# Kernel tuning notes

Hardware: AMD Instinct MI355X
Metric: run time of the kernel (lower is better)

Reference implementation:

```python
import jax, jax.numpy as jnp
import numpy as np

L = 65536   # sequence length (keys/values)
D = 512     # embed dim (hardcoded in source)
H = 4       # heads
HD = 128    # head dim

def _ln(x, g, b):
    m = jnp.mean(x, -1, keepdims=True)
    v = jnp.var(x, -1, keepdims=True)
    return (x - m) * jax.lax.rsqrt(v + 1e-5) * g + b

def setup_inputs() -> dict:
    key = jax.random.key(0)
    ks = jax.random.split(key, 6)
    s = 0.02
    return {
        "x": jax.random.normal(ks[0], (L, D), jnp.float32),
        "w_in": jax.random.normal(ks[1], (3 * D, D), jnp.float32) * s,
        "b_in": jnp.zeros((3 * D,), jnp.float32),
        "w_out": jax.random.normal(ks[2], (D, D), jnp.float32) * s,
        "b_out": jnp.zeros((D,), jnp.float32),
        "w1": jax.random.normal(ks[3], (D, D), jnp.float32) * s,
        "b1": jnp.zeros((D,), jnp.float32),
        "w2": jax.random.normal(ks[4], (D, D), jnp.float32) * s,
        "b2": jnp.zeros((D,), jnp.float32),
        "g1": jnp.ones((D,), jnp.float32),
        "be1": jnp.zeros((D,), jnp.float32),
        "g2": jnp.ones((D,), jnp.float32),
        "be2": jnp.zeros((D,), jnp.float32),
    }

def reference(x, w_in, b_in, w_out, b_out, w1, b1, w2, b2, g1, be1, g2, be2):
    xn = _ln(x, g1, be1)                               # [L, D]
    q = xn[:1] @ w_in[:D].T + b_in[:D]                 # [1, D] single-row query
    k = xn @ w_in[D:2 * D].T + b_in[D:2 * D]           # [L, D]
    v = xn @ w_in[2 * D:].T + b_in[2 * D:]             # [L, D]
    qh = q.reshape(H, HD)                              # [H, HD]
    kh = k.reshape(L, H, HD)
    vh = v.reshape(L, H, HD)
    scores = jnp.einsum('hd,lhd->hl', qh, kh) * (1.0 / np.sqrt(HD))  # [H, L]
    attn = jax.nn.softmax(scores, axis=-1)
    o = jnp.einsum('hl,lhd->hd', attn, vh).reshape(1, D)             # [1, D]
    o = o @ w_out.T + b_out
    y = x[:1] + o                                      # residual keeps only row 0
    yn = _ln(y, g2, be2)
    h = jax.nn.relu(yn @ w1.T + b1)
    return y + h @ w2.T + b2                           # [1, D]
```

## Files before the change

### kernel.cpp

```cpp
#include <hip/hip_runtime.h>
#include <math.h>

#define LL 65536
#define DD 512
#define NH 4
#define HDIM 128


__device__ __forceinline__ float dot4(float4 a, float4 b) {
    return a.x * b.x + a.y * b.y + a.z * b.z + a.w * b.w;
}
__device__ __forceinline__ float wred(float v) {
#pragma unroll
    for (int m = 32; m; m >>= 1) v += __shfl_xor(v, m, 64);
    return v;
}
__device__ __forceinline__ float4 f4fma(float4 acc, float s, float4 v) {
    acc.x += s * v.x; acc.y += s * v.y; acc.z += s * v.z; acc.w += s * v.w;
    return acc;
}
__device__ __forceinline__ float4 f4add(float4 a, float4 b) {
    a.x += b.x; a.y += b.y; a.z += b.z; a.w += b.w; return a;
}
__device__ __forceinline__ float4 f4muls(float4 a, float4 g, float s) {
    a.x *= g.x * s; a.y *= g.y * s; a.z *= g.z * s; a.w *= g.w * s; return a;
}
__device__ __forceinline__ float hsum4(float4 a) { return a.x + a.y + a.z + a.w; }
__device__ __forceinline__ float4 lnrm4(float4 v, float m, float r, float4 g, float4 b) {
    float4 o;
    o.x = (v.x - m) * r * g.x + b.x; o.y = (v.y - m) * r * g.y + b.y;
    o.z = (v.z - m) * r * g.z + b.z; o.w = (v.w - m) * r * g.w + b.w;
    return o;
}
__device__ __forceinline__ float4 caff4(float4 c, float inv, float w2t, float4 g, float4 b) {
    float4 o;
    o.x = g.x * (c.x * inv - w2t) + b.x; o.y = g.y * (c.y * inv - w2t) + b.y;
    o.z = g.z * (c.z * inv - w2t) + b.z; o.w = g.w * (c.w * inv - w2t) + b.w;
    return o;
}

__global__ __launch_bounds__(256) void kA1(const float* __restrict__ x,
                                           const float* __restrict__ w_in,
                                           const float* __restrict__ b_in,
                                           const float* __restrict__ g1,
                                           const float* __restrict__ be1,
                                           float* __restrict__ ws) {
    int lane = threadIdx.x & 63;
    int j = blockIdx.x * 4 + (threadIdx.x >> 6);
    const float4* x4 = (const float4*)x;
    float4 a = x4[lane], b = x4[64 + lane];
    float ps = hsum4(a) + hsum4(b);
    float pss = dot4(a, a) + dot4(b, b);
    ps = wred(ps); pss = wred(pss);
    float m = ps * (1.f / 512.f);
    float r = rsqrtf(pss * (1.f / 512.f) - m * m + 1e-5f);
    const float4* g4 = (const float4*)g1;
    const float4* bb4 = (const float4*)be1;
    float4 xna = lnrm4(a, m, r, g4[lane], bb4[lane]);
    float4 xnb = lnrm4(b, m, r, g4[64 + lane], bb4[64 + lane]);
    const float4* wr = (const float4*)(w_in + (size_t)j * DD);
    float acc = dot4(wr[lane], xna) + dot4(wr[64 + lane], xnb);
    acc = wred(acc);
    if (lane == 0) ws[j] = acc + b_in[j];
}

__global__ __launch_bounds__(512) void kA2(const float* __restrict__ w_in,
                                           float* __restrict__ ws) {
    __shared__ float qh[32];
    int bi = blockIdx.x, tid = threadIdx.x;
    int h = bi >> 2, c = bi & 3;
    if (tid < 32) qh[tid] = ws[h * HDIM + c * 32 + tid];
    if (tid < 128) ws[9216 + bi * 128 + tid] = 0.f;
    __syncthreads();
    const float* wk = w_in + (size_t)(DD + h * HDIM + c * 32) * DD + tid;
    float acc = 0.f;
#pragma unroll
    for (int d = 0; d < 32; ++d) acc += qh[d] * wk[(size_t)d * DD];
    ws[1024 + c * 2048 + h * 512 + tid] = acc;
}

__global__ __launch_bounds__(512) void kB(const float* __restrict__ x,
                                          const float* __restrict__ g1,
                                          float* __restrict__ ws) {
    __shared__ float lds[16384];
    int tid = threadIdx.x, lane = tid & 63, w = tid >> 6;
    const float4* p4 = (const float4*)(ws + 1024);
    const float4* g4 = (const float4*)g1;
    const float scale = 0.088388347648318447f;
    float4 ga = g4[lane], gb = g4[64 + lane];
    float4 qa[4], qb[4];
    float qs[4];
#pragma unroll
    for (int h = 0; h < 4; ++h) {
        float4 sa = f4add(f4add(p4[h * 128 + lane], p4[512 + h * 128 + lane]),
                          f4add(p4[1024 + h * 128 + lane], p4[1536 + h * 128 + lane]));
        float4 sb = f4add(f4add(p4[h * 128 + 64 + lane], p4[512 + h * 128 + 64 + lane]),
                          f4add(p4[1024 + h * 128 + 64 + lane], p4[1536 + h * 128 + 64 + lane]));
        qa[h] = f4muls(sa, ga, scale);
        qb[h] = f4muls(sb, gb, scale);
        qs[h] = wred(hsum4(qa[h]) + hsum4(qb[h]));
    }
    float sm[4], w2a[4];
    float4 Wa[4], Wb[4];
#pragma unroll
    for (int h = 0; h < 4; ++h) {
        sm[h] = 0.f; w2a[h] = 0.f;
        Wa[h] = make_float4(0.f, 0.f, 0.f, 0.f);
        Wb[h] = make_float4(0.f, 0.f, 0.f, 0.f);
    }
    size_t row0 = ((size_t)blockIdx.x * 8 + w) * 16;
    const float4* xb = (const float4*)x + row0 * 128;
    float4 nxa = xb[lane], nxc = xb[64 + lane];
    for (int r = 0; r < 16; ++r) {
        float4 xa = nxa, xc = nxc;
        if (r < 15) { nxa = xb[(r + 1) * 128 + lane]; nxc = xb[(r + 1) * 128 + 64 + lane]; }
        float ps = hsum4(xa) + hsum4(xc);
        float pss = dot4(xa, xa) + dot4(xc, xc);
        float p0 = dot4(xa, qa[0]) + dot4(xc, qb[0]);
        float p1 = dot4(xa, qa[1]) + dot4(xc, qb[1]);
        float p2 = dot4(xa, qa[2]) + dot4(xc, qb[2]);
        float p3 = dot4(xa, qa[3]) + dot4(xc, qb[3]);
        ps = wred(ps); pss = wred(pss);
        p0 = wred(p0); p1 = wred(p1); p2 = wred(p2); p3 = wred(p3);
        float m = ps * (1.f / 512.f);
        float rr = rsqrtf(pss * (1.f / 512.f) - m * m + 1e-5f);
        float rm = rr * m;
        float pd[4] = {p0, p1, p2, p3};
#pragma unroll
        for (int h = 0; h < 4; ++h) {
            float s = rr * pd[h] - rm * qs[h];
            float p = __expf(s);
            sm[h] += p;
            w2a[h] += p * rm;
            float pr = p * rr;
            Wa[h] = f4fma(Wa[h], pr, xa);
            Wb[h] = f4fma(Wb[h], pr, xc);
        }
    }
    if (lane == 0) {
#pragma unroll
        for (int h = 0; h < 4; ++h) {
            lds[w * 4 + h] = sm[h];
            lds[32 + w * 4 + h] = w2a[h];
        }
    }
    __syncthreads();
    if (tid < 8) {
        int h = tid & 3;
        float a = 0.f;
        if (tid < 4) {
            for (int ww = 0; ww < 8; ++ww) a += lds[ww * 4 + h];
            ws[16384 + blockIdx.x * 4 + h] = a;
        } else {
            for (int ww = 0; ww < 8; ++ww) a += lds[32 + ww * 4 + h];
            ws[18432 + blockIdx.x * 4 + h] = a;
        }
    }
    __syncthreads();
    float4* lw4 = (float4*)(lds + w * 2048);
#pragma unroll
    for (int h = 0; h < 4; ++h) {
        lw4[h * 128 + lane] = Wa[h];
        lw4[h * 128 + 64 + lane] = Wb[h];
    }
    __syncthreads();
    float* Wout = ws + 20480 + (size_t)blockIdx.x * 2048;
    for (int i = tid; i < 2048; i += 512) {
        float a = lds[i] + lds[2048 + i] + lds[4096 + i] + lds[6144 + i] +
                  lds[8192 + i] + lds[10240 + i] + lds[12288 + i] + lds[14336 + i];
        Wout[i] = a;
    }
}

__global__ __launch_bounds__(256) void kC1(float* __restrict__ ws) {
    int g = blockIdx.x * 256 + threadIdx.x;
    int col = g & 2047, chunk = g >> 11;
    const float* Wb = ws + 20480 + (size_t)chunk * 32 * 2048 + col;
    float acc = 0.f;
#pragma unroll 8
    for (int b = 0; b < 32; ++b) acc += Wb[(size_t)b * 2048];
    atomicAdd(&ws[9216 + col], acc);
}

__global__ __launch_bounds__(256) void kD1(const float* __restrict__ w_in,
                                           const float* __restrict__ b_in,
                                           const float* __restrict__ g1,
                                           const float* __restrict__ be1,
                                           float* __restrict__ ws) {
    __shared__ float sred[16];
    int tid = threadIdx.x, lane = tid & 63, w = tid >> 6;
    int j = blockIdx.x * 4 + w;
    int h = j >> 7;
    float s1 = ws[16384 + tid * 4 + h] + ws[16384 + (tid + 256) * 4 + h];
    float s2 = ws[18432 + tid * 4 + h] + ws[18432 + (tid + 256) * 4 + h];
    s1 = wred(s1); s2 = wred(s2);
    if (lane == 0) { sred[w * 2] = s1; sred[w * 2 + 1] = s2; }
    __syncthreads();
    float smg = sred[0] + sred[2] + sred[4] + sred[6];
    float w2g = sred[1] + sred[3] + sred[5] + sred[7];
    float inv = 1.f / smg;
    float w2t = w2g * inv;
    const float4* cr = (const float4*)(ws + 9216 + h * 512);
    const float4* g14 = (const float4*)g1;
    const float4* be14 = (const float4*)be1;
    float4 ca = caff4(cr[lane], inv, w2t, g14[lane], be14[lane]);
    float4 cb = caff4(cr[64 + lane], inv, w2t, g14[64 + lane], be14[64 + lane]);
    const float4* wr = (const float4*)(w_in + (size_t)(2 * DD + j) * DD);
    float acc = dot4(wr[lane], ca) + dot4(wr[64 + lane], cb);
    acc = wred(acc);
    if (lane == 0) ws[11264 + j] = acc + b_in[2 * DD + j];
}

__global__ __launch_bounds__(256) void kD2(const float* __restrict__ x,
                                           const float* __restrict__ w_out,
                                           const float* __restrict__ b_out,
                                           float* __restrict__ ws) {
    int lane = threadIdx.x & 63;
    int j = blockIdx.x * 4 + (threadIdx.x >> 6);
    const float4* wr = (const float4*)(w_out + (size_t)j * DD);
    const float4* o4 = (const float4*)(ws + 11264);
    float acc = dot4(wr[lane], o4[lane]) + dot4(wr[64 + lane], o4[64 + lane]);
    acc = wred(acc);
    if (lane == 0) ws[11776 + j] = x[j] + acc + b_out[j];
}

__global__ __launch_bounds__(256) void kD3(const float* __restrict__ w1,
                                           const float* __restrict__ b1,
                                           const float* __restrict__ g2,
                                           const float* __restrict__ be2,
                                           float* __restrict__ ws) {
    int lane = threadIdx.x & 63;
    int j = blockIdx.x * 4 + (threadIdx.x >> 6);
    const float4* y4 = (const float4*)(ws + 11776);
    float4 ya = y4[lane], yb = y4[64 + lane];
    float ps = hsum4(ya) + hsum4(yb);
    float pss = dot4(ya, ya) + dot4(yb, yb);
    ps = wred(ps); pss = wred(pss);
    float m2 = ps * (1.f / 512.f);
    float r2 = rsqrtf(pss * (1.f / 512.f) - m2 * m2 + 1e-5f);
    const float4* g4 = (const float4*)g2;
    const float4* b4 = (const float4*)be2;
    float4 yna = lnrm4(ya, m2, r2, g4[lane], b4[lane]);
    float4 ynb = lnrm4(yb, m2, r2, g4[64 + lane], b4[64 + lane]);
    const float4* wr = (const float4*)(w1 + (size_t)j * DD);
    float acc = dot4(wr[lane], yna) + dot4(wr[64 + lane], ynb);
    acc = wred(acc);
    if (lane == 0) ws[12288 + j] = fmaxf(acc + b1[j], 0.f);
}

__global__ __launch_bounds__(256) void kD4(const float* __restrict__ w2,
                                           const float* __restrict__ b2,
                                           const float* __restrict__ ws,
                                           float* __restrict__ out) {
    int lane = threadIdx.x & 63;
    int j = blockIdx.x * 4 + (threadIdx.x >> 6);
    const float4* h4 = (const float4*)(ws + 12288);
    const float4* wr = (const float4*)(w2 + (size_t)j * DD);
    float acc = dot4(wr[lane], h4[lane]) + dot4(wr[64 + lane], h4[64 + lane]);
    acc = wred(acc);
    if (lane == 0) out[j] = ws[11776 + j] + acc + b2[j];
}

extern "C" void kernel_launch(void* const* d_in, const int* in_sizes, int n_in,
                              void* d_out, int out_size, void* d_ws, size_t ws_size,
                              hipStream_t stream) {
    (void)in_sizes; (void)n_in; (void)out_size; (void)ws_size;
    const float* x = (const float*)d_in[0];
    const float* w_in = (const float*)d_in[1];
    const float* b_in = (const float*)d_in[2];
    const float* w_out = (const float*)d_in[3];
    const float* b_out = (const float*)d_in[4];
    const float* w1 = (const float*)d_in[5];
    const float* b1 = (const float*)d_in[6];
    const float* w2 = (const float*)d_in[7];
    const float* b2 = (const float*)d_in[8];
    const float* g1 = (const float*)d_in[9];
    const float* be1 = (const float*)d_in[10];
    const float* g2 = (const float*)d_in[11];
    const float* be2 = (const float*)d_in[12];
    float* ws = (float*)d_ws;
    float* out = (float*)d_out;

    hipLaunchKernelGGL(kA1, dim3(128), dim3(256), 0, stream, x, w_in, b_in, g1, be1, ws);
    hipLaunchKernelGGL(kA2, dim3(16), dim3(512), 0, stream, w_in, ws);
    hipLaunchKernelGGL(kB, dim3(512), dim3(512), 0, stream, x, g1, ws);
    hipLaunchKernelGGL(kC1, dim3(128), dim3(256), 0, stream, ws);
    hipLaunchKernelGGL(kD1, dim3(128), dim3(256), 0, stream, w_in, b_in, g1, be1, ws);
    hipLaunchKernelGGL(kD2, dim3(128), dim3(256), 0, stream, x, w_out, b_out, ws);
    hipLaunchKernelGGL(kD3, dim3(128), dim3(256), 0, stream, w1, b1, g2, be2, ws);
    hipLaunchKernelGGL(kD4, dim3(128), dim3(256), 0, stream, w2, b2, ws, out);
}
```

Measured before the change: 239.1 us.

## Fuse all stages into one cooperative kernel with grid-wide syncs

Replaces the eight separate kernel launches with one cooperative kernel of 256 blocks that uses grid.sync between phases. The first phase now computes q and the q·Wk product in just 4 blocks. The main streaming pass does 32 rows per warp with a two-deep prefetch. Partial sums are reduced through LDS and atomics into 8 slot buffers, which removes the separate cross-block reduction kernel. This cuts launch and inter-kernel gaps, at the cost of grid barriers, heavier serial work in a few blocks for the first phase, and atomic contention.

Measured after the change: 417.5 us. 74.6% more time.

```diff
diff --git a/kernel.cpp b/kernel.cpp
--- a/kernel.cpp
+++ b/kernel.cpp
@@ -1,10 +1,10 @@
 #include <hip/hip_runtime.h>
+#include <hip/hip_cooperative_groups.h>
 #include <math.h>
 
-#define LL 65536
+namespace cg = cooperative_groups;
+
 #define DD 512
-#define NH 4
-#define HDIM 128
 
 
 __device__ __forceinline__ float dot4(float4 a, float4 b) {
@@ -21,9 +21,6 @@
 }
 __device__ __forceinline__ float4 f4add(float4 a, float4 b) {
     a.x += b.x; a.y += b.y; a.z += b.z; a.w += b.w; return a;
-}
-__device__ __forceinline__ float4 f4muls(float4 a, float4 g, float s) {
-    a.x *= g.x * s; a.y *= g.y * s; a.z *= g.z * s; a.w *= g.w * s; return a;
 }
 __device__ __forceinline__ float hsum4(float4 a) { return a.x + a.y + a.z + a.w; }
 __device__ __forceinline__ float4 lnrm4(float4 v, float m, float r, float4 g, float4 b) {
@@ -39,226 +36,222 @@
     return o;
 }
 
-__global__ __launch_bounds__(256) void kA1(const float* __restrict__ x,
-                                           const float* __restrict__ w_in,
-                                           const float* __restrict__ b_in,
-                                           const float* __restrict__ g1,
-                                           const float* __restrict__ be1,
-                                           float* __restrict__ ws) {
-    int lane = threadIdx.x & 63;
-    int j = blockIdx.x * 4 + (threadIdx.x >> 6);
-    const float4* x4 = (const float4*)x;
-    float4 a = x4[lane], b = x4[64 + lane];
-    float ps = hsum4(a) + hsum4(b);
-    float pss = dot4(a, a) + dot4(b, b);
-    ps = wred(ps); pss = wred(pss);
-    float m = ps * (1.f / 512.f);
-    float r = rsqrtf(pss * (1.f / 512.f) - m * m + 1e-5f);
-    const float4* g4 = (const float4*)g1;
-    const float4* bb4 = (const float4*)be1;
-    float4 xna = lnrm4(a, m, r, g4[lane], bb4[lane]);
-    float4 xnb = lnrm4(b, m, r, g4[64 + lane], bb4[64 + lane]);
-    const float4* wr = (const float4*)(w_in + (size_t)j * DD);
-    float acc = dot4(wr[lane], xna) + dot4(wr[64 + lane], xnb);
-    acc = wred(acc);
-    if (lane == 0) ws[j] = acc + b_in[j];
-}
-
-__global__ __launch_bounds__(512) void kA2(const float* __restrict__ w_in,
-                                           float* __restrict__ ws) {
-    __shared__ float qh[32];
-    int bi = blockIdx.x, tid = threadIdx.x;
-    int h = bi >> 2, c = bi & 3;
-    if (tid < 32) qh[tid] = ws[h * HDIM + c * 32 + tid];
-    if (tid < 128) ws[9216 + bi * 128 + tid] = 0.f;
-    __syncthreads();
-    const float* wk = w_in + (size_t)(DD + h * HDIM + c * 32) * DD + tid;
-    float acc = 0.f;
-#pragma unroll
-    for (int d = 0; d < 32; ++d) acc += qh[d] * wk[(size_t)d * DD];
-    ws[1024 + c * 2048 + h * 512 + tid] = acc;
-}
-
-__global__ __launch_bounds__(512) void kB(const float* __restrict__ x,
-                                          const float* __restrict__ g1,
-                                          float* __restrict__ ws) {
-    __shared__ float lds[16384];
+__global__ __launch_bounds__(512, 2) void kMega(
+    const float* __restrict__ x,
+    const float* __restrict__ w_in, const float* __restrict__ b_in,
+    const float* __restrict__ w_out, const float* __restrict__ b_out,
+    const float* __restrict__ w1, const float* __restrict__ b1,
+    const float* __restrict__ w2, const float* __restrict__ b2,
+    const float* __restrict__ g1, const float* __restrict__ be1,
+    const float* __restrict__ g2, const float* __restrict__ be2,
+    float* __restrict__ ws, float* __restrict__ out)
+{
+    __shared__ float lds[8192];
+    __shared__ float lstats[64];
+    cg::grid_group grid = cg::this_grid();
     int tid = threadIdx.x, lane = tid & 63, w = tid >> 6;
-    const float4* p4 = (const float4*)(ws + 1024);
-    const float4* g4 = (const float4*)g1;
+    int bid = blockIdx.x;
     const float scale = 0.088388347648318447f;
-    float4 ga = g4[lane], gb = g4[64 + lane];
-    float4 qa[4], qb[4];
-    float qs[4];
-#pragma unroll
-    for (int h = 0; h < 4; ++h) {
-        float4 sa = f4add(f4add(p4[h * 128 + lane], p4[512 + h * 128 + lane]),
-                          f4add(p4[1024 + h * 128 + lane], p4[1536 + h * 128 + lane]));
-        float4 sb = f4add(f4add(p4[h * 128 + 64 + lane], p4[512 + h * 128 + 64 + lane]),
-                          f4add(p4[1024 + h * 128 + 64 + lane], p4[1536 + h * 128 + 64 + lane]));
-        qa[h] = f4muls(sa, ga, scale);
-        qb[h] = f4muls(sb, gb, scale);
-        qs[h] = wred(hsum4(qa[h]) + hsum4(qb[h]));
-    }
-    float sm[4], w2a[4];
-    float4 Wa[4], Wb[4];
-#pragma unroll
-    for (int h = 0; h < 4; ++h) {
-        sm[h] = 0.f; w2a[h] = 0.f;
-        Wa[h] = make_float4(0.f, 0.f, 0.f, 0.f);
-        Wb[h] = make_float4(0.f, 0.f, 0.f, 0.f);
-    }
-    size_t row0 = ((size_t)blockIdx.x * 8 + w) * 16;
-    const float4* xb = (const float4*)x + row0 * 128;
-    float4 nxa = xb[lane], nxc = xb[64 + lane];
-    for (int r = 0; r < 16; ++r) {
-        float4 xa = nxa, xc = nxc;
-        if (r < 15) { nxa = xb[(r + 1) * 128 + lane]; nxc = xb[(r + 1) * 128 + 64 + lane]; }
-        float ps = hsum4(xa) + hsum4(xc);
-        float pss = dot4(xa, xa) + dot4(xc, xc);
-        float p0 = dot4(xa, qa[0]) + dot4(xc, qb[0]);
-        float p1 = dot4(xa, qa[1]) + dot4(xc, qb[1]);
-        float p2 = dot4(xa, qa[2]) + dot4(xc, qb[2]);
-        float p3 = dot4(xa, qa[3]) + dot4(xc, qb[3]);
-        ps = wred(ps); pss = wred(pss);
-        p0 = wred(p0); p1 = wred(p1); p2 = wred(p2); p3 = wred(p3);
+
+    if (bid < 4) {
+        int h = bid;
+        const float4* x4 = (const float4*)x;
+        float4 a = x4[lane], b = x4[64 + lane];
+        float ps = wred(hsum4(a) + hsum4(b));
+        float pss = wred(dot4(a, a) + dot4(b, b));
         float m = ps * (1.f / 512.f);
-        float rr = rsqrtf(pss * (1.f / 512.f) - m * m + 1e-5f);
-        float rm = rr * m;
-        float pd[4] = {p0, p1, p2, p3};
+        float r = rsqrtf(pss * (1.f / 512.f) - m * m + 1e-5f);
+        const float4* g4 = (const float4*)g1;
+        const float4* bb4 = (const float4*)be1;
+        float4 xna = lnrm4(a, m, r, g4[lane], bb4[lane]);
+        float4 xnb = lnrm4(b, m, r, g4[64 + lane], bb4[64 + lane]);
+        const float4* wr = (const float4*)(w_in + (size_t)(h * 128 + w * 16) * DD);
+        float4 wa = wr[lane], wb = wr[64 + lane];
+        for (int i = 0; i < 16; ++i) {
+            float4 ca = wa, cb = wb;
+            if (i < 15) { wa = wr[(i + 1) * 128 + lane]; wb = wr[(i + 1) * 128 + 64 + lane]; }
+            float acc = wred(dot4(ca, xna) + dot4(cb, xnb));
+            if (lane == 0) lds[w * 16 + i] = acc + b_in[h * 128 + w * 16 + i];
+        }
+        __syncthreads();
+        const float* wk = w_in + (size_t)(DD + h * 128) * DD + tid;
+        float acc = 0.f;
+#pragma unroll 16
+        for (int d = 0; d < 128; ++d) acc += lds[d] * wk[(size_t)d * DD];
+        float qg = acc * scale * g1[tid];
+        ws[h * 512 + tid] = qg;
+        float s = wred(qg);
+        if (lane == 0) lds[4096 + w] = s;
+        __syncthreads();
+        if (tid == 0) {
+            float t = 0.f;
+            for (int ww = 0; ww < 8; ++ww) t += lds[4096 + ww];
+            ws[2048 + h] = t;
+        }
+    } else if (bid < 36) {
+        ws[4096 + (bid - 4) * 512 + tid] = 0.f;
+        if (bid == 35 && tid < 192) ws[2176 + tid] = 0.f;
+    }
+    grid.sync();
+
+    {
+        const float4* qkg4 = (const float4*)ws;
+        float4 qa[4], qb[4];
+        float qs[4];
 #pragma unroll
         for (int h = 0; h < 4; ++h) {
-            float s = rr * pd[h] - rm * qs[h];
-            float p = __expf(s);
-            sm[h] += p;
-            w2a[h] += p * rm;
-            float pr = p * rr;
-            Wa[h] = f4fma(Wa[h], pr, xa);
-            Wb[h] = f4fma(Wb[h], pr, xc);
-        }
-    }
-    if (lane == 0) {
+            qa[h] = qkg4[h * 128 + lane];
+            qb[h] = qkg4[h * 128 + 64 + lane];
+            qs[h] = ws[2048 + h];
+        }
+        float sm[4], w2a[4];
+        float4 Wa[4], Wb[4];
 #pragma unroll
         for (int h = 0; h < 4; ++h) {
-            lds[w * 4 + h] = sm[h];
-            lds[32 + w * 4 + h] = w2a[h];
-        }
-    }
-    __syncthreads();
-    if (tid < 8) {
-        int h = tid & 3;
-        float a = 0.f;
-        if (tid < 4) {
-            for (int ww = 0; ww < 8; ++ww) a += lds[ww * 4 + h];
-            ws[16384 + blockIdx.x * 4 + h] = a;
-        } else {
-            for (int ww = 0; ww < 8; ++ww) a += lds[32 + ww * 4 + h];
-            ws[18432 + blockIdx.x * 4 + h] = a;
-        }
-    }
-    __syncthreads();
-    float4* lw4 = (float4*)(lds + w * 2048);
-#pragma unroll
-    for (int h = 0; h < 4; ++h) {
-        lw4[h * 128 + lane] = Wa[h];
-        lw4[h * 128 + 64 + lane] = Wb[h];
-    }
-    __syncthreads();
-    float* Wout = ws + 20480 + (size_t)blockIdx.x * 2048;
-    for (int i = tid; i < 2048; i += 512) {
-        float a = lds[i] + lds[2048 + i] + lds[4096 + i] + lds[6144 + i] +
-                  lds[8192 + i] + lds[10240 + i] + lds[12288 + i] + lds[14336 + i];
-        Wout[i] = a;
-    }
-}
-
-__global__ __launch_bounds__(256) void kC1(float* __restrict__ ws) {
-    int g = blockIdx.x * 256 + threadIdx.x;
-    int col = g & 2047, chunk = g >> 11;
-    const float* Wb = ws + 20480 + (size_t)chunk * 32 * 2048 + col;
-    float acc = 0.f;
-#pragma unroll 8
-    for (int b = 0; b < 32; ++b) acc += Wb[(size_t)b * 2048];
-    atomicAdd(&ws[9216 + col], acc);
-}
-
-__global__ __launch_bounds__(256) void kD1(const float* __restrict__ w_in,
-                                           const float* __restrict__ b_in,
-                                           const float* __restrict__ g1,
-                                           const float* __restrict__ be1,
-                                           float* __restrict__ ws) {
-    __shared__ float sred[16];
-    int tid = threadIdx.x, lane = tid & 63, w = tid >> 6;
-    int j = blockIdx.x * 4 + w;
-    int h = j >> 7;
-    float s1 = ws[16384 + tid * 4 + h] + ws[16384 + (tid + 256) * 4 + h];
-    float s2 = ws[18432 + tid * 4 + h] + ws[18432 + (tid + 256) * 4 + h];
-    s1 = wred(s1); s2 = wred(s2);
-    if (lane == 0) { sred[w * 2] = s1; sred[w * 2 + 1] = s2; }
-    __syncthreads();
-    float smg = sred[0] + sred[2] + sred[4] + sred[6];
-    float w2g = sred[1] + sred[3] + sred[5] + sred[7];
-    float inv = 1.f / smg;
-    float w2t = w2g * inv;
-    const float4* cr = (const float4*)(ws + 9216 + h * 512);
-    const float4* g14 = (const float4*)g1;
-    const float4* be14 = (const float4*)be1;
-    float4 ca = caff4(cr[lane], inv, w2t, g14[lane], be14[lane]);
-    float4 cb = caff4(cr[64 + lane], inv, w2t, g14[64 + lane], be14[64 + lane]);
-    const float4* wr = (const float4*)(w_in + (size_t)(2 * DD + j) * DD);
-    float acc = dot4(wr[lane], ca) + dot4(wr[64 + lane], cb);
-    acc = wred(acc);
-    if (lane == 0) ws[11264 + j] = acc + b_in[2 * DD + j];
-}
-
-__global__ __launch_bounds__(256) void kD2(const float* __restrict__ x,
-                                           const float* __restrict__ w_out,
-                                           const float* __restrict__ b_out,
-                                           float* __restrict__ ws) {
-    int lane = threadIdx.x & 63;
-    int j = blockIdx.x * 4 + (threadIdx.x >> 6);
-    const float4* wr = (const float4*)(w_out + (size_t)j * DD);
-    const float4* o4 = (const float4*)(ws + 11264);
-    float acc = dot4(wr[lane], o4[lane]) + dot4(wr[64 + lane], o4[64 + lane]);
-    acc = wred(acc);
-    if (lane == 0) ws[11776 + j] = x[j] + acc + b_out[j];
-}
-
-__global__ __launch_bounds__(256) void kD3(const float* __restrict__ w1,
-                                           const float* __restrict__ b1,
-                                           const float* __restrict__ g2,
-                                           const float* __restrict__ be2,
-                                           float* __restrict__ ws) {
-    int lane = threadIdx.x & 63;
-    int j = blockIdx.x * 4 + (threadIdx.x >> 6);
-    const float4* y4 = (const float4*)(ws + 11776);
-    float4 ya = y4[lane], yb = y4[64 + lane];
-    float ps = hsum4(ya) + hsum4(yb);
-    float pss = dot4(ya, ya) + dot4(yb, yb);
-    ps = wred(ps); pss = wred(pss);
-    float m2 = ps * (1.f / 512.f);
-    float r2 = rsqrtf(pss * (1.f / 512.f) - m2 * m2 + 1e-5f);
-    const float4* g4 = (const float4*)g2;
-    const float4* b4 = (const float4*)be2;
-    float4 yna = lnrm4(ya, m2, r2, g4[lane], b4[lane]);
-    float4 ynb = lnrm4(yb, m2, r2, g4[64 + lane], b4[64 + lane]);
-    const float4* wr = (const float4*)(w1 + (size_t)j * DD);
-    float acc = dot4(wr[lane], yna) + dot4(wr[64 + lane], ynb);
-    acc = wred(acc);
-    if (lane == 0) ws[12288 + j] = fmaxf(acc + b1[j], 0.f);
-}
-
-__global__ __launch_bounds__(256) void kD4(const float* __restrict__ w2,
-                                           const float* __restrict__ b2,
-                                           const float* __restrict__ ws,
-                                           float* __restrict__ out) {
-    int lane = threadIdx.x & 63;
-    int j = blockIdx.x * 4 + (threadIdx.x >> 6);
-    const float4* h4 = (const float4*)(ws + 12288);
-    const float4* wr = (const float4*)(w2 + (size_t)j * DD);
-    float acc = dot4(wr[lane], h4[lane]) + dot4(wr[64 + lane], h4[64 + lane]);
-    acc = wred(acc);
-    if (lane == 0) out[j] = ws[11776 + j] + acc + b2[j];
+            sm[h] = 0.f; w2a[h] = 0.f;
+            Wa[h] = make_float4(0.f, 0.f, 0.f, 0.f);
+            Wb[h] = make_float4(0.f, 0.f, 0.f, 0.f);
+        }
+        size_t row0 = ((size_t)bid * 8 + w) * 32;
+        const float4* xb = (const float4*)x + row0 * 128;
+        float4 a0 = xb[lane],       c0 = xb[64 + lane];
+        float4 a1 = xb[128 + lane], c1 = xb[192 + lane];
+        for (int r = 0; r < 32; ++r) {
+            float4 xa = a0, xc = c0;
+            a0 = a1; c0 = c1;
+            if (r < 30) { a1 = xb[(r + 2) * 128 + lane]; c1 = xb[(r + 2) * 128 + 64 + lane]; }
+            float ps = hsum4(xa) + hsum4(xc);
+            float pss = dot4(xa, xa) + dot4(xc, xc);
+            float p0 = dot4(xa, qa[0]) + dot4(xc, qb[0]);
+            float p1 = dot4(xa, qa[1]) + dot4(xc, qb[1]);
+            float p2 = dot4(xa, qa[2]) + dot4(xc, qb[2]);
+            float p3 = dot4(xa, qa[3]) + dot4(xc, qb[3]);
+            ps = wred(ps); pss = wred(pss);
+            p0 = wred(p0); p1 = wred(p1); p2 = wred(p2); p3 = wred(p3);
+            float m = ps * (1.f / 512.f);
+            float rr = rsqrtf(pss * (1.f / 512.f) - m * m + 1e-5f);
+            float rm = rr * m;
+            float pd[4] = {p0, p1, p2, p3};
+#pragma unroll
+            for (int h = 0; h < 4; ++h) {
+                float s = rr * pd[h] - rm * qs[h];
+                float p = __expf(s);
+                sm[h] += p;
+                w2a[h] += p * rm;
+                float pr = p * rr;
+                Wa[h] = f4fma(Wa[h], pr, xa);
+                Wb[h] = f4fma(Wb[h], pr, xc);
+            }
+        }
+        if (lane == 0) {
+#pragma unroll
+            for (int i = 0; i < 4; ++i) { lstats[w * 8 + i] = sm[i]; lstats[w * 8 + 4 + i] = w2a[i]; }
+        }
+        if (w >= 4) {
+            float4* dst = (float4*)(lds + (w - 4) * 2048);
+#pragma unroll
+            for (int h = 0; h < 4; ++h) { dst[h * 128 + lane] = Wa[h]; dst[h * 128 + 64 + lane] = Wb[h]; }
+        }
+        __syncthreads();
+        if (w < 4) {
+            const float4* srcp = (const float4*)(lds + w * 2048);
+#pragma unroll
+            for (int h = 0; h < 4; ++h) {
+                Wa[h] = f4add(Wa[h], srcp[h * 128 + lane]);
+                Wb[h] = f4add(Wb[h], srcp[h * 128 + 64 + lane]);
+            }
+        }
+        __syncthreads();
+        if (w == 2 || w == 3) {
+            float4* dst = (float4*)(lds + (w - 2) * 2048);
+#pragma unroll
+            for (int h = 0; h < 4; ++h) { dst[h * 128 + lane] = Wa[h]; dst[h * 128 + 64 + lane] = Wb[h]; }
+        }
+        __syncthreads();
+        if (w < 2) {
+            const float4* srcp = (const float4*)(lds + w * 2048);
+            float* base = ws + 4096 + (size_t)(bid & 7) * 2048;
+#pragma unroll
+            for (int h = 0; h < 4; ++h) {
+                Wa[h] = f4add(Wa[h], srcp[h * 128 + lane]);
+                Wb[h] = f4add(Wb[h], srcp[h * 128 + 64 + lane]);
+                int cA = h * 512 + 4 * lane;
+                atomicAdd(base + cA + 0, Wa[h].x); atomicAdd(base + cA + 1, Wa[h].y);
+                atomicAdd(base + cA + 2, Wa[h].z); atomicAdd(base + cA + 3, Wa[h].w);
+                int cB = h * 512 + 256 + 4 * lane;
+                atomicAdd(base + cB + 0, Wb[h].x); atomicAdd(base + cB + 1, Wb[h].y);
+                atomicAdd(base + cB + 2, Wb[h].z); atomicAdd(base + cB + 3, Wb[h].w);
+            }
+        }
+        if (tid < 8) {
+            float a = 0.f;
+            for (int ww = 0; ww < 8; ++ww) a += lstats[ww * 8 + tid];
+            atomicAdd(&ws[2176 + (bid & 7) * 16 + tid], a);
+        }
+    }
+    grid.sync();
+
+    if (bid < 64) {
+        int j = bid * 8 + w;
+        int h = j >> 7;
+        float smg = 0.f, w2g = 0.f;
+#pragma unroll
+        for (int c = 0; c < 8; ++c) {
+            smg += ws[2176 + c * 16 + h];
+            w2g += ws[2176 + c * 16 + 4 + h];
+        }
+        float inv = 1.f / smg, w2t = w2g * inv;
+        float4 cra = make_float4(0.f, 0.f, 0.f, 0.f), crb = cra;
+#pragma unroll
+        for (int c = 0; c < 8; ++c) {
+            const float4* cr = (const float4*)(ws + 4096 + c * 2048 + h * 512);
+            cra = f4add(cra, cr[lane]);
+            crb = f4add(crb, cr[64 + lane]);
+        }
+        const float4* g14 = (const float4*)g1;
+        const float4* be14 = (const float4*)be1;
+        float4 ca = caff4(cra, inv, w2t, g14[lane], be14[lane]);
+        float4 cb = caff4(crb, inv, w2t, g14[64 + lane], be14[64 + lane]);
+        const float4* wr = (const float4*)(w_in + (size_t)(2 * DD + j) * DD);
+        float acc = wred(dot4(wr[lane], ca) + dot4(wr[64 + lane], cb));
+        if (lane == 0) ws[2560 + j] = acc + b_in[2 * DD + j];
+    }
+    grid.sync();
+
+    if (bid < 64) {
+        int j = bid * 8 + w;
+        const float4* wr = (const float4*)(w_out + (size_t)j * DD);
+        const float4* o4 = (const float4*)(ws + 2560);
+        float acc = wred(dot4(wr[lane], o4[lane]) + dot4(wr[64 + lane], o4[64 + lane]));
+        if (lane == 0) ws[3072 + j] = x[j] + acc + b_out[j];
+    }
+    grid.sync();
+
+    if (bid < 64) {
+        int j = bid * 8 + w;
+        const float4* y4 = (const float4*)(ws + 3072);
+        float4 ya = y4[lane], yb = y4[64 + lane];
+        float ps = wred(hsum4(ya) + hsum4(yb));
+        float pss = wred(dot4(ya, ya) + dot4(yb, yb));
+        float m2 = ps * (1.f / 512.f);
+        float r2 = rsqrtf(pss * (1.f / 512.f) - m2 * m2 + 1e-5f);
+        const float4* g4 = (const float4*)g2;
+        const float4* b4 = (const float4*)be2;
+        float4 yna = lnrm4(ya, m2, r2, g4[lane], b4[lane]);
+        float4 ynb = lnrm4(yb, m2, r2, g4[64 + lane], b4[64 + lane]);
+        const float4* wr = (const float4*)(w1 + (size_t)j * DD);
+        float acc = wred(dot4(wr[lane], yna) + dot4(wr[64 + lane], ynb));
+        if (lane == 0) ws[3584 + j] = fmaxf(acc + b1[j], 0.f);
+    }
+    grid.sync();
+
+    if (bid < 64) {
+        int j = bid * 8 + w;
+        const float4* h4 = (const float4*)(ws + 3584);
+        const float4* wr = (const float4*)(w2 + (size_t)j * DD);
+        float acc = wred(dot4(wr[lane], h4[lane]) + dot4(wr[64 + lane], h4[64 + lane]));
+        if (lane == 0) out[j] = ws[3072 + j] + acc + b2[j];
+    }
 }
 
 extern "C" void kernel_launch(void* const* d_in, const int* in_sizes, int n_in,
@@ -281,12 +274,11 @@
     float* ws = (float*)d_ws;
     float* out = (float*)d_out;
 
-    hipLaunchKernelGGL(kA1, dim3(128), dim3(256), 0, stream, x, w_in, b_in, g1, be1, ws);
-    hipLaunchKernelGGL(kA2, dim3(16), dim3(512), 0, stream, w_in, ws);
-    hipLaunchKernelGGL(kB, dim3(512), dim3(512), 0, stream, x, g1, ws);
-    hipLaunchKernelGGL(kC1, dim3(128), dim3(256), 0, stream, ws);
-    hipLaunchKernelGGL(kD1, dim3(128), dim3(256), 0, stream, w_in, b_in, g1, be1, ws);
-    hipLaunchKernelGGL(kD2, dim3(128), dim3(256), 0, stream, x, w_out, b_out, ws);
-    hipLaunchKernelGGL(kD3, dim3(128), dim3(256), 0, stream, w1, b1, g2, be2, ws);
-    hipLaunchKernelGGL(kD4, dim3(128), dim3(256), 0, stream, w2, b2, ws, out);
-}
+    void* args[] = {
+        (void*)&x, (void*)&w_in, (void*)&b_in, (void*)&w_out, (void*)&b_out,
+        (void*)&w1, (void*)&b1, (void*)&w2, (void*)&b2,
+        (void*)&g1, (void*)&be1, (void*)&g2, (void*)&be2,
+        (void*)&ws, (void*)&out
+    };
+    hipLaunchCooperativeKernel((const void*)kMega, dim3(256), dim3(512), args, 0, stream);
+}
```

## Fuse query projection kernels and replace partial-sum pass with atomic accumulation

Applied to the files above, without the earlier changes.

Merges the query projection and q·Wk folding into one kernel, where each block computes its 32 query elements locally. The separate kC1 reduction kernel is removed: kB blocks now atomically add their partial sums and weighted-value accumulators into 16 replicated copies, and kD1 sums those copies. This drops two launches and the large per-block workspace write and read-back. In exchange it adds atomic contention and makes the floating-point summation order nondeterministic.

Measured after the change: 236.6 us, median of 2. Within noise of the previous version (-1.0%).

```diff
diff --git a/kernel.cpp b/kernel.cpp
--- a/kernel.cpp
+++ b/kernel.cpp
@@ -1,10 +1,7 @@
 #include <hip/hip_runtime.h>
 #include <math.h>
 
-#define LL 65536
 #define DD 512
-#define NH 4
-#define HDIM 128
 
 
 __device__ __forceinline__ float dot4(float4 a, float4 b) {
@@ -39,44 +36,42 @@
     return o;
 }
 
-__global__ __launch_bounds__(256) void kA1(const float* __restrict__ x,
-                                           const float* __restrict__ w_in,
-                                           const float* __restrict__ b_in,
-                                           const float* __restrict__ g1,
-                                           const float* __restrict__ be1,
-                                           float* __restrict__ ws) {
-    int lane = threadIdx.x & 63;
-    int j = blockIdx.x * 4 + (threadIdx.x >> 6);
+__global__ __launch_bounds__(512) void kA(const float* __restrict__ x,
+                                          const float* __restrict__ w_in,
+                                          const float* __restrict__ b_in,
+                                          const float* __restrict__ g1,
+                                          const float* __restrict__ be1,
+                                          float* __restrict__ ws) {
+    __shared__ float qh[32];
+    int bi = blockIdx.x, tid = threadIdx.x, lane = tid & 63, w = tid >> 6;
+    int h = bi >> 2, c = bi & 3;
+    {
+        float4 z = make_float4(0.f, 0.f, 0.f, 0.f);
+        ((float4*)(ws + 8448))[bi * 512 + tid] = z;
+        if (bi == 0 && tid < 128) ws[8192 + tid] = 0.f;
+    }
     const float4* x4 = (const float4*)x;
     float4 a = x4[lane], b = x4[64 + lane];
-    float ps = hsum4(a) + hsum4(b);
-    float pss = dot4(a, a) + dot4(b, b);
-    ps = wred(ps); pss = wred(pss);
+    float ps = wred(hsum4(a) + hsum4(b));
+    float pss = wred(dot4(a, a) + dot4(b, b));
     float m = ps * (1.f / 512.f);
     float r = rsqrtf(pss * (1.f / 512.f) - m * m + 1e-5f);
     const float4* g4 = (const float4*)g1;
     const float4* bb4 = (const float4*)be1;
     float4 xna = lnrm4(a, m, r, g4[lane], bb4[lane]);
     float4 xnb = lnrm4(b, m, r, g4[64 + lane], bb4[64 + lane]);
-    const float4* wr = (const float4*)(w_in + (size_t)j * DD);
-    float acc = dot4(wr[lane], xna) + dot4(wr[64 + lane], xnb);
-    acc = wred(acc);
-    if (lane == 0) ws[j] = acc + b_in[j];
-}
-
-__global__ __launch_bounds__(512) void kA2(const float* __restrict__ w_in,
-                                           float* __restrict__ ws) {
-    __shared__ float qh[32];
-    int bi = blockIdx.x, tid = threadIdx.x;
-    int h = bi >> 2, c = bi & 3;
-    if (tid < 32) qh[tid] = ws[h * HDIM + c * 32 + tid];
-    if (tid < 128) ws[9216 + bi * 128 + tid] = 0.f;
-    __syncthreads();
-    const float* wk = w_in + (size_t)(DD + h * HDIM + c * 32) * DD + tid;
+    int j0 = h * 128 + c * 32;
+    const float4* wr = (const float4*)(w_in + (size_t)(j0 + w * 4) * DD);
+    for (int i = 0; i < 4; ++i) {
+        float acc = wred(dot4(wr[i * 128 + lane], xna) + dot4(wr[i * 128 + 64 + lane], xnb));
+        if (lane == 0) qh[w * 4 + i] = acc + b_in[j0 + w * 4 + i];
+    }
+    __syncthreads();
+    const float* wk = w_in + (size_t)(DD + j0) * DD + tid;
     float acc = 0.f;
 #pragma unroll
     for (int d = 0; d < 32; ++d) acc += qh[d] * wk[(size_t)d * DD];
-    ws[1024 + c * 2048 + h * 512 + tid] = acc;
+    ws[c * 2048 + h * 512 + tid] = acc;
 }
 
 __global__ __launch_bounds__(512) void kB(const float* __restrict__ x,
@@ -84,7 +79,7 @@
                                           float* __restrict__ ws) {
     __shared__ float lds[16384];
     int tid = threadIdx.x, lane = tid & 63, w = tid >> 6;
-    const float4* p4 = (const float4*)(ws + 1024);
+    const float4* p4 = (const float4*)ws;
     const float4* g4 = (const float4*)g1;
     const float scale = 0.088388347648318447f;
     float4 ga = g4[lane], gb = g4[64 + lane];
@@ -137,6 +132,7 @@
             Wb[h] = f4fma(Wb[h], pr, xc);
         }
     }
+    int copy = blockIdx.x & 15;
     if (lane == 0) {
 #pragma unroll
         for (int h = 0; h < 4; ++h) {
@@ -150,10 +146,10 @@
         float a = 0.f;
         if (tid < 4) {
             for (int ww = 0; ww < 8; ++ww) a += lds[ww * 4 + h];
-            ws[16384 + blockIdx.x * 4 + h] = a;
+            atomicAdd(&ws[8192 + copy * 4 + h], a);
         } else {
             for (int ww = 0; ww < 8; ++ww) a += lds[32 + ww * 4 + h];
-            ws[18432 + blockIdx.x * 4 + h] = a;
+            atomicAdd(&ws[8256 + copy * 4 + h], a);
         }
     }
     __syncthreads();
@@ -164,22 +160,12 @@
         lw4[h * 128 + 64 + lane] = Wb[h];
     }
     __syncthreads();
-    float* Wout = ws + 20480 + (size_t)blockIdx.x * 2048;
+    float* cdst = ws + 8448 + (size_t)copy * 2048;
     for (int i = tid; i < 2048; i += 512) {
         float a = lds[i] + lds[2048 + i] + lds[4096 + i] + lds[6144 + i] +
                   lds[8192 + i] + lds[10240 + i] + lds[12288 + i] + lds[14336 + i];
-        Wout[i] = a;
-    }
-}
-
-__global__ __launch_bounds__(256) void kC1(float* __restrict__ ws) {
-    int g = blockIdx.x * 256 + threadIdx.x;
-    int col = g & 2047, chunk = g >> 11;
-    const float* Wb = ws + 20480 + (size_t)chunk * 32 * 2048 + col;
-    float acc = 0.f;
-#pragma unroll 8
-    for (int b = 0; b < 32; ++b) acc += Wb[(size_t)b * 2048];
-    atomicAdd(&ws[9216 + col], acc);
+        atomicAdd(cdst + i, a);
+    }
 }
 
 __global__ __launch_bounds__(256) void kD1(const float* __restrict__ w_in,
@@ -187,28 +173,30 @@
                                            const float* __restrict__ g1,
                                            const float* __restrict__ be1,
                                            float* __restrict__ ws) {
-    __shared__ float sred[16];
     int tid = threadIdx.x, lane = tid & 63, w = tid >> 6;
     int j = blockIdx.x * 4 + w;
     int h = j >> 7;
-    float s1 = ws[16384 + tid * 4 + h] + ws[16384 + (tid + 256) * 4 + h];
-    float s2 = ws[18432 + tid * 4 + h] + ws[18432 + (tid + 256) * 4 + h];
-    s1 = wred(s1); s2 = wred(s2);
-    if (lane == 0) { sred[w * 2] = s1; sred[w * 2 + 1] = s2; }
-    __syncthreads();
-    float smg = sred[0] + sred[2] + sred[4] + sred[6];
-    float w2g = sred[1] + sred[3] + sred[5] + sred[7];
-    float inv = 1.f / smg;
-    float w2t = w2g * inv;
-    const float4* cr = (const float4*)(ws + 9216 + h * 512);
+    float smg = 0.f, w2g = 0.f;
+#pragma unroll
+    for (int c = 0; c < 16; ++c) {
+        smg += ws[8192 + c * 4 + h];
+        w2g += ws[8256 + c * 4 + h];
+    }
+    float inv = 1.f / smg, w2t = w2g * inv;
+    float4 cra = make_float4(0.f, 0.f, 0.f, 0.f), crb = cra;
+#pragma unroll
+    for (int c = 0; c < 16; ++c) {
+        const float4* cr = (const float4*)(ws + 8448 + c * 2048 + h * 512);
+        cra = f4add(cra, cr[lane]);
+        crb = f4add(crb, cr[64 + lane]);
+    }
     const float4* g14 = (const float4*)g1;
     const float4* be14 = (const float4*)be1;
-    float4 ca = caff4(cr[lane], inv, w2t, g14[lane], be14[lane]);
-    float4 cb = caff4(cr[64 + lane], inv, w2t, g14[64 + lane], be14[64 + lane]);
+    float4 ca = caff4(cra, inv, w2t, g14[lane], be14[lane]);
+    float4 cb = caff4(crb, inv, w2t, g14[64 + lane], be14[64 + lane]);
     const float4* wr = (const float4*)(w_in + (size_t)(2 * DD + j) * DD);
-    float acc = dot4(wr[lane], ca) + dot4(wr[64 + lane], cb);
-    acc = wred(acc);
-    if (lane == 0) ws[11264 + j] = acc + b_in[2 * DD + j];
+    float acc = wred(dot4(wr[lane], ca) + dot4(wr[64 + lane], cb));
+    if (lane == 0) ws[41216 + j] = acc + b_in[2 * DD + j];
 }
 
 __global__ __launch_bounds__(256) void kD2(const float* __restrict__ x,
@@ -218,10 +206,9 @@
     int lane = threadIdx.x & 63;
     int j = blockIdx.x * 4 + (threadIdx.x >> 6);
     const float4* wr = (const float4*)(w_out + (size_t)j * DD);
-    const float4* o4 = (const float4*)(ws + 11264);
-    float acc = dot4(wr[lane], o4[lane]) + dot4(wr[64 + lane], o4[64 + lane]);
-    acc = wred(acc);
-    if (lane == 0) ws[11776 + j] = x[j] + acc + b_out[j];
+    const float4* o4 = (const float4*)(ws + 41216);
+    float acc = wred(dot4(wr[lane], o4[lane]) + dot4(wr[64 + lane], o4[64 + lane]));
+    if (lane == 0) ws[41728 + j] = x[j] + acc + b_out[j];
 }
 
 __global__ __launch_bounds__(256) void kD3(const float* __restrict__ w1,
@@ -231,11 +218,10 @@
                                            float* __restrict__ ws) {
     int lane = threadIdx.x & 63;
     int j = blockIdx.x * 4 + (threadIdx.x >> 6);
-    const float4* y4 = (const float4*)(ws + 11776);
+    const float4* y4 = (const float4*)(ws + 41728);
     float4 ya = y4[lane], yb = y4[64 + lane];
-    float ps = hsum4(ya) + hsum4(yb);
-    float pss = dot4(ya, ya) + dot4(yb, yb);
-    ps = wred(ps); pss = wred(pss);
+    float ps = wred(hsum4(ya) + hsum4(yb));
+    float pss = wred(dot4(ya, ya) + dot4(yb, yb));
     float m2 = ps * (1.f / 512.f);
     float r2 = rsqrtf(pss * (1.f / 512.f) - m2 * m2 + 1e-5f);
     const float4* g4 = (const float4*)g2;
@@ -243,9 +229,8 @@
     float4 yna = lnrm4(ya, m2, r2, g4[lane], b4[lane]);
     float4 ynb = lnrm4(yb, m2, r2, g4[64 + lane], b4[64 + lane]);
     const float4* wr = (const float4*)(w1 + (size_t)j * DD);
-    float acc = dot4(wr[lane], yna) + dot4(wr[64 + lane], ynb);
-    acc = wred(acc);
-    if (lane == 0) ws[12288 + j] = fmaxf(acc + b1[j], 0.f);
+    float acc = wred(dot4(wr[lane], yna) + dot4(wr[64 + lane], ynb));
+    if (lane == 0) ws[42240 + j] = fmaxf(acc + b1[j], 0.f);
 }
 
 __global__ __launch_bounds__(256) void kD4(const float* __restrict__ w2,
@@ -254,11 +239,10 @@
                                            float* __restrict__ out) {
     int lane = threadIdx.x & 63;
     int j = blockIdx.x * 4 + (threadIdx.x >> 6);
-    const float4* h4 = (const float4*)(ws + 12288);
+    const float4* h4 = (const float4*)(ws + 42240);
     const float4* wr = (const float4*)(w2 + (size_t)j * DD);
-    float acc = dot4(wr[lane], h4[lane]) + dot4(wr[64 + lane], h4[64 + lane]);
-    acc = wred(acc);
-    if (lane == 0) out[j] = ws[11776 + j] + acc + b2[j];
+    float acc = wred(dot4(wr[lane], h4[lane]) + dot4(wr[64 + lane], h4[64 + lane]));
+    if (lane == 0) out[j] = ws[41728 + j] + acc + b2[j];
 }
 
 extern "C" void kernel_launch(void* const* d_in, const int* in_sizes, int n_in,
@@ -281,10 +265,8 @@
     float* ws = (float*)d_ws;
     float* out = (float*)d_out;
 
-    hipLaunchKernelGGL(kA1, dim3(128), dim3(256), 0, stream, x, w_in, b_in, g1, be1, ws);
-    hipLaunchKernelGGL(kA2, dim3(16), dim3(512), 0, stream, w_in, ws);
+    hipLaunchKernelGGL(kA, dim3(16), dim3(512), 0, stream, x, w_in, b_in, g1, be1, ws);
     hipLaunchKernelGGL(kB, dim3(512), dim3(512), 0, stream, x, g1, ws);
-    hipLaunchKernelGGL(kC1, dim3(128), dim3(256), 0, stream, ws);
     hipLaunchKernelGGL(kD1, dim3(128), dim3(256), 0, stream, w_in, b_in, g1, be1, ws);
     hipLaunchKernelGGL(kD2, dim3(128), dim3(256), 0, stream, x, w_out, b_out, ws);
     hipLaunchKernelGGL(kD3, dim3(128), dim3(256), 0, stream, w1, b1, g2, be2, ws);
```
